# Optimization experiments

Hardware: AMD Instinct MI355X
Metric: run time of the kernel (lower is better)

Reference implementation:

```python
import jax, jax.numpy as jnp
import numpy as np

TOP_K = 2  # k in TopKGate


def setup_inputs() -> dict:
    key = jax.random.key(0)
    k1, k2, k3 = jax.random.split(key, 3)
    B, S, H, E = 4, 2048, 1024, 8
    hidden_states = jax.random.normal(k1, (B, S, H), dtype=jnp.float32)
    Wg = jax.random.normal(k2, (H, E), dtype=jnp.float32) * (H ** -0.5)
    We = jax.random.normal(k3, (E, H, H), dtype=jnp.float32) * (H ** -0.5)
    be = jnp.zeros((E, H), dtype=jnp.float32)
    return {"hidden_states": hidden_states, "Wg": Wg, "We": We, "be": be}


def reference(hidden_states, Wg, We, be):
    # hidden_states: [B, S, H]; Wg: [H, E]; We: [E, H, H]; be: [E, H]
    B, S, H = hidden_states.shape
    T = B * S
    x = hidden_states.reshape(T, H)

    # TopKGate: linear gate -> softmax -> top-k -> renormalize combine weights
    probs = jax.nn.softmax(x @ Wg, axis=-1)              # [T, E]
    top_vals, top_idx = jax.lax.top_k(probs, TOP_K)     # [T, K]
    gates = top_vals / jnp.sum(top_vals, axis=-1, keepdims=True)

    # Experts: run each token through each expert Linear, then gather top-k
    expert_out = jnp.einsum('th,ehd->etd', x, We) + be[:, None, :]  # [E, T, H]
    tok = jnp.arange(T)[:, None]                         # [T, 1]
    sel = expert_out[top_idx, tok, :]                    # [T, K, H]

    # Weighted combine over top-k experts
    out = jnp.sum(gates[..., None] * sel, axis=1)        # [T, H]
    return out.reshape(B, S, H)
```

## Files before the change

### kernel.cpp

```cpp
#include <hip/hip_runtime.h>
#include <hip/hip_bf16.h>

#define H 1024
#define NEXP 8
#define T_TOK 8192
#define CAP 8192
#define TM 128
#define TN 128
#define CNTSTRIDE 32

typedef __bf16 bf16x8 __attribute__((ext_vector_type(8)));
typedef __bf16 bf16x4 __attribute__((ext_vector_type(4)));
typedef float f32x4 __attribute__((ext_vector_type(4)));

__device__ __forceinline__ void async16(void* lds, const void* g) {
    __builtin_amdgcn_global_load_lds(
        (const __attribute__((address_space(1))) void*)g,
        (__attribute__((address_space(3))) void*)lds, 16, 0, 0);
}

__global__ __launch_bounds__(256) void moe_prep(
    const float* __restrict__ We, __bf16* __restrict__ WeT,
    const float* __restrict__ x, const float* __restrict__ Wg,
    __bf16* __restrict__ Xb, int* __restrict__ cnt,
    int* __restrict__ ltok,
    int* __restrict__ tsel, float* __restrict__ tgate) {
    __shared__ __align__(16) char smem[NEXP * H * 4];
    __shared__ __align__(16) float fin[4][8];
    __shared__ int   sE[8];
    __shared__ float sG[8];
    __shared__ int   lcnt[NEXP], lbase[NEXP], lslot[8];
    const int tid  = threadIdx.x;
    const int lane = tid & 63;
    const int wave = tid >> 6;

    if (blockIdx.x >= 2048) {
        float (*t)[65] = (float(*)[65])smem;
        const int tt = blockIdx.x - 2048;
        const int e  = tt >> 8;
        const int d0 = ((tt >> 4) & 15) * 64;
        const int h0 = (tt & 15) * 64;
        const int tx = tid & 15;
        const int ty = tid >> 4;
        const float* src = We + ((size_t)e << 20);
        __bf16* dst = WeT + ((size_t)e << 20);
#pragma unroll
        for (int p = 0; p < 4; ++p) {
            const int row = p * 16 + ty;
            const float4 v = *(const float4*)(src + (size_t)(h0 + row) * H + d0 + tx * 4);
            t[row][tx * 4 + 0] = v.x; t[row][tx * 4 + 1] = v.y;
            t[row][tx * 4 + 2] = v.z; t[row][tx * 4 + 3] = v.w;
        }
        __syncthreads();
#pragma unroll
        for (int qq = 0; qq < 2; ++qq) {
            const int q = tid + qq * 256;
            const int drow = q >> 3;
            const int seg  = q & 7;
            bf16x8 o;
#pragma unroll
            for (int i = 0; i < 8; ++i) o[i] = (__bf16)t[seg * 8 + i][drow];
            *(bf16x8*)(dst + (size_t)(d0 + drow) * H + h0 + seg * 8) = o;
        }
        return;
    }

    float (*wgT)[H] = (float(*)[H])smem;
    const int t = blockIdx.x * 4 + wave;

#pragma unroll
    for (int k = 0; k < 8; ++k) {
        const int q = k * 256 + tid;
        const float4 f = ((const float4*)Wg)[q];
        const int h  = q >> 1;
        const int e0 = (q & 1) * 4;
        wgT[e0 + 0][h] = f.x; wgT[e0 + 1][h] = f.y;
        wgT[e0 + 2][h] = f.z; wgT[e0 + 3][h] = f.w;
    }

    const float* xr = x + (size_t)t * H;
    float4 xv[4];
#pragma unroll
    for (int c = 0; c < 4; ++c)
        xv[c] = *(const float4*)(xr + c * 256 + lane * 4);

    __bf16* xbr = Xb + (size_t)t * H;
#pragma unroll
    for (int c = 0; c < 4; ++c) {
        bf16x4 xo;
        xo[0] = (__bf16)xv[c].x; xo[1] = (__bf16)xv[c].y;
        xo[2] = (__bf16)xv[c].z; xo[3] = (__bf16)xv[c].w;
        *(bf16x4*)(xbr + c * 256 + lane * 4) = xo;
    }

    __syncthreads();

    float a[NEXP];
#pragma unroll
    for (int e = 0; e < NEXP; ++e) a[e] = 0.f;
#pragma unroll
    for (int e = 0; e < NEXP; ++e) {
#pragma unroll
        for (int c = 0; c < 4; ++c) {
            const float4 wv = *(const float4*)&wgT[e][c * 256 + lane * 4];
            a[e] += xv[c].x * wv.x + xv[c].y * wv.y + xv[c].z * wv.z + xv[c].w * wv.w;
        }
    }
    if (tid < NEXP) lcnt[tid] = 0;
    __syncthreads();

    float* rw = (float*)smem + wave * 512;
#pragma unroll
    for (int e = 0; e < NEXP; ++e) rw[e * 64 + lane] = a[e];
    const int eL = lane >> 3, l8 = lane & 7;
    const float4 p0 = *(const float4*)&rw[eL * 64 + l8 * 8];
    const float4 p1 = *(const float4*)&rw[eL * 64 + l8 * 8 + 4];
    float s = ((p0.x + p0.y) + (p0.z + p0.w)) + ((p1.x + p1.y) + (p1.z + p1.w));
    s += __shfl_xor(s, 1, 64);
    s += __shfl_xor(s, 2, 64);
    s += __shfl_xor(s, 4, 64);
    if (l8 == 0) fin[wave][eL] = s;
    const float4 f0 = *(const float4*)&fin[wave][0];
    const float4 f1 = *(const float4*)&fin[wave][4];
    const float av[NEXP] = {f0.x, f0.y, f0.z, f0.w, f1.x, f1.y, f1.z, f1.w};

    int i0 = 0;
#pragma unroll
    for (int e = 1; e < NEXP; ++e) if (av[e] > av[i0]) i0 = e;
    int i1 = (i0 == 0) ? 1 : 0;
#pragma unroll
    for (int e = 0; e < NEXP; ++e) if (e != i0 && av[e] > av[i1]) i1 = e;
    const float ex = __expf(av[i1] - av[i0]);
    const float g0 = 1.f / (1.f + ex);
    const float g1 = ex / (1.f + ex);
    if (lane == 0) {
        sE[wave * 2] = i0; sE[wave * 2 + 1] = i1;
        sG[wave * 2] = g0; sG[wave * 2 + 1] = g1;
    }
    __syncthreads();
    if (tid < 8) lslot[tid] = atomicAdd(&lcnt[sE[tid]], 1);
    __syncthreads();
    if (tid < NEXP) lbase[tid] = lcnt[tid] ? atomicAdd(&cnt[tid * CNTSTRIDE], lcnt[tid]) : 0;
    __syncthreads();
    if (tid < 8) {
        const int e = sE[tid];
        const int sl = lbase[e] + lslot[tid];
        const int tt2 = blockIdx.x * 4 + (tid >> 1);
        ltok[e * CAP + sl] = tt2;
        tsel[tt2 * 2 + (tid & 1)]  = e * CAP + sl;
        tgate[tt2 * 2 + (tid & 1)] = sG[tid];
    }
}

__global__ __launch_bounds__(256) void moe_gemm(
    const __bf16* __restrict__ Xb, const __bf16* __restrict__ WeT,
    const float* __restrict__ be, const int* __restrict__ cnt,
    const int* __restrict__ ltok,
    __bf16* __restrict__ Eout) {
    const int e  = blockIdx.x & 7;
    const int nt = (blockIdx.x >> 3) & 7;
    const int mt = blockIdx.x >> 6;
    const int ne = cnt[e * CNTSTRIDE];
    const int m0 = mt * TM;
    if (m0 >= ne) return;
    const int n0 = nt * TN;
    int off = 0;
    for (int i2 = 0; i2 < e; ++i2) off += cnt[i2 * CNTSTRIDE];

    __shared__ __align__(16) __bf16 smem[4 * 4096];
    __bf16* Al  = smem;
    __bf16* Al2 = smem + 4096;
    __bf16* Bl  = smem + 8192;
    __bf16* Bl2 = smem + 12288;
    __shared__ int tokL[TM];

    const int tid = threadIdx.x;
    const int lane = tid & 63;
    const int wave = tid >> 6;

    if (tid < TM) {
        const int gi = m0 + tid;
        tokL[tid] = (gi < ne) ? ltok[e * CAP + gi] : 0;
    }
    __syncthreads();

    const __bf16* Bt = WeT + ((size_t)e << 20);
    const int qr = lane >> 4;
    const int rr = lane & 15;
    const int wr = (wave >> 1) * 64;
    const int wc = (wave & 1) * 64;

    f32x4 acc[4][4];
    const f32x4 z = {0.f, 0.f, 0.f, 0.f};
#pragma unroll
    for (int i = 0; i < 4; ++i)
#pragma unroll
        for (int j = 0; j < 4; ++j) acc[i][j] = z;

    const int c0 = tid, c1 = tid + 256;
    const int ar0 = c0 >> 2, ak0 = (((c0 & 3) ^ ((c0 >> 3) & 3)) * 8);
    const int ar1 = c1 >> 2, ak1 = (((c1 & 3) ^ ((c1 >> 3) & 3)) * 8);
    const size_t arow0 = (size_t)tokL[ar0] * H;
    const size_t arow1 = (size_t)tokL[ar1] * H;
    const size_t brow0 = (size_t)(n0 + ar0) * H;
    const size_t brow1 = (size_t)(n0 + ar1) * H;

    for (int k0 = 0; k0 < H; k0 += 64) {
        async16(&Al [c0 * 8], Xb + arow0 + k0 + ak0);
        async16(&Al [c1 * 8], Xb + arow1 + k0 + ak1);
        async16(&Al2[c0 * 8], Xb + arow0 + k0 + 32 + ak0);
        async16(&Al2[c1 * 8], Xb + arow1 + k0 + 32 + ak1);
        async16(&Bl [c0 * 8], Bt + brow0 + k0 + ak0);
        async16(&Bl [c1 * 8], Bt + brow1 + k0 + ak1);
        async16(&Bl2[c0 * 8], Bt + brow0 + k0 + 32 + ak0);
        async16(&Bl2[c1 * 8], Bt + brow1 + k0 + 32 + ak1);
        __syncthreads();
        {
            bf16x8 af[4], bfr[4];
#pragma unroll
            for (int i = 0; i < 4; ++i) {
                const int ra = wr + i * 16 + rr;
                af[i] = *(const bf16x8*)&Al[ra * 32 + ((qr ^ ((ra >> 1) & 3)) * 8)];
            }
#pragma unroll
            for (int j = 0; j < 4; ++j) {
                const int rb = wc + j * 16 + rr;
                bfr[j] = *(const bf16x8*)&Bl[rb * 32 + ((qr ^ ((rb >> 1) & 3)) * 8)];
            }
#pragma unroll
            for (int i = 0; i < 4; ++i)
#pragma unroll
                for (int j = 0; j < 4; ++j)
                    acc[i][j] = __builtin_amdgcn_mfma_f32_16x16x32_bf16(af[i], bfr[j], acc[i][j], 0, 0, 0);
        }
        {
            bf16x8 af[4], bfr[4];
#pragma unroll
            for (int i = 0; i < 4; ++i) {
                const int ra = wr + i * 16 + rr;
                af[i] = *(const bf16x8*)&Al2[ra * 32 + ((qr ^ ((ra >> 1) & 3)) * 8)];
            }
#pragma unroll
            for (int j = 0; j < 4; ++j) {
                const int rb = wc + j * 16 + rr;
                bfr[j] = *(const bf16x8*)&Bl2[rb * 32 + ((qr ^ ((rb >> 1) & 3)) * 8)];
            }
#pragma unroll
            for (int i = 0; i < 4; ++i)
#pragma unroll
                for (int j = 0; j < 4; ++j)
                    acc[i][j] = __builtin_amdgcn_mfma_f32_16x16x32_bf16(af[i], bfr[j], acc[i][j], 0, 0, 0);
        }
        __syncthreads();
    }

    float bev[4];
#pragma unroll
    for (int j = 0; j < 4; ++j) bev[j] = be[e * H + n0 + wc + j * 16 + rr];

    __bf16* Cw = smem + wave * 4096;
#pragma unroll
    for (int i = 0; i < 4; ++i) {
#pragma unroll
        for (int reg = 0; reg < 4; ++reg) {
            const int row = i * 16 + qr * 4 + reg;
            const int key = (row & 7) * 8;
#pragma unroll
            for (int j = 0; j < 4; ++j) {
                const int c = j * 16 + rr;
                Cw[row * 64 + (c ^ key)] = (__bf16)(acc[i][j][reg] + bev[j]);
            }
        }
    }
    const int lrr = lane & 7, lrg = lane >> 3;
#pragma unroll
    for (int p = 0; p < 8; ++p) {
        const int row = p * 8 + lrg;
        const int rglob = m0 + wr + row;
        if (rglob < ne) {
            const int idx8 = ((lrr ^ (row & 7)) * 8);
            const bf16x8 v = *(const bf16x8*)&Cw[row * 64 + idx8];
            *(bf16x8*)(Eout + (size_t)(off + rglob) * H + n0 + wc + lrr * 8) = v;
        }
    }
}

__global__ __launch_bounds__(256) void moe_combine(
    const __bf16* __restrict__ Eout, const int* __restrict__ cnt,
    const int* __restrict__ tsel, const float* __restrict__ tgate,
    float* __restrict__ out) {
    __shared__ int offs[NEXP];
    if (threadIdx.x < NEXP) {
        int o = 0;
        for (int i = 0; i < (int)threadIdx.x; ++i) o += cnt[i * CNTSTRIDE];
        offs[threadIdx.x] = o;
    }
    __syncthreads();
    const int wave = threadIdx.x >> 6, lane = threadIdx.x & 63;
    const int t = blockIdx.x * 4 + wave;
    const int sel0 = tsel[t * 2],  sel1 = tsel[t * 2 + 1];
    const float g0 = tgate[t * 2], g1  = tgate[t * 2 + 1];
    const int e0 = sel0 >> 13, s0 = sel0 & (CAP - 1);
    const int e1 = sel1 >> 13, s1 = sel1 & (CAP - 1);
    const __bf16* r0 = Eout + (size_t)(offs[e0] + s0) * H;
    const __bf16* r1 = Eout + (size_t)(offs[e1] + s1) * H;
    float* orow = out + (size_t)t * H;
#pragma unroll
    for (int c = 0; c < 2; ++c) {
        const int d = c * 512 + lane * 8;
        const bf16x8 a = *(const bf16x8*)(r0 + d);
        const bf16x8 b = *(const bf16x8*)(r1 + d);
        float4 o0, o1;
        o0.x = g0 * (float)a[0] + g1 * (float)b[0];
        o0.y = g0 * (float)a[1] + g1 * (float)b[1];
        o0.z = g0 * (float)a[2] + g1 * (float)b[2];
        o0.w = g0 * (float)a[3] + g1 * (float)b[3];
        o1.x = g0 * (float)a[4] + g1 * (float)b[4];
        o1.y = g0 * (float)a[5] + g1 * (float)b[5];
        o1.z = g0 * (float)a[6] + g1 * (float)b[6];
        o1.w = g0 * (float)a[7] + g1 * (float)b[7];
        *(float4*)(orow + d)     = o0;
        *(float4*)(orow + d + 4) = o1;
    }
}

extern "C" void kernel_launch(void* const* d_in, const int* in_sizes, int n_in,
                              void* d_out, int out_size, void* d_ws, size_t ws_size,
                              hipStream_t stream) {
    const float* x  = (const float*)d_in[0];
    const float* Wg = (const float*)d_in[1];
    const float* We = (const float*)d_in[2];
    const float* be = (const float*)d_in[3];
    float* out = (float*)d_out;

    char* ws = (char*)d_ws;
    __bf16* Xb   = (__bf16*)ws;
    __bf16* WeT  = (__bf16*)(ws + ((size_t)16 << 20));
    __bf16* Eout = (__bf16*)(ws + ((size_t)32 << 20));
    char*   meta = ws + ((size_t)64 << 20);
    int*    cnt  = (int*)meta;
    int*    ltok = (int*)(meta + 1024);
    int*    tsel = (int*)(meta + 1024 + (size_t)NEXP * CAP * 8);
    float*  tgat = (float*)(meta + 1024 + (size_t)NEXP * CAP * 8 + (size_t)T_TOK * 8);

    hipMemsetAsync(cnt, 0, NEXP * CNTSTRIDE * sizeof(int), stream);

    moe_prep<<<4096, 256, 0, stream>>>(We, WeT, x, Wg, Xb, cnt, ltok, tsel, tgat);
    moe_gemm<<<8 * 8 * (T_TOK / TM), 256, 0, stream>>>(Xb, WeT, be, cnt, ltok, Eout);
    moe_combine<<<T_TOK / 4, 256, 0, stream>>>(Eout, cnt, tsel, tgat, out);
}
```

Before: 182.2 us.

## Pipeline expert GEMM K-loop with triple-buffered async LDS loads

Replaces the load-then-sync-then-compute K loop (64-wide steps, two sync barriers per step) with a three-stage ring of 32-wide K tiles. Global-to-LDS loads for tile k+2 are issued while tile k is computed, and explicit vmcnt waits with a single raw barrier per step replace __syncthreads. This is meant to hide global load latency behind MFMA work. In exchange it uses more LDS (48KB vs 32KB), which may reduce occupancy, and it doubles the number of loop iterations and barriers.

```diff
diff --git a/kernel.cpp b/kernel.cpp
--- a/kernel.cpp
+++ b/kernel.cpp
@@ -18,6 +18,13 @@
         (const __attribute__((address_space(1))) void*)g,
         (__attribute__((address_space(3))) void*)lds, 16, 0, 0);
 }
+
+__device__ __forceinline__ void bar() {
+    asm volatile("" ::: "memory");
+    __builtin_amdgcn_s_barrier();
+    asm volatile("" ::: "memory");
+}
+#define VMCNT(n) asm volatile("s_waitcnt vmcnt(" #n ")" ::: "memory")
 
 __global__ __launch_bounds__(256) void moe_prep(
     const float* __restrict__ We, __bf16* __restrict__ WeT,
@@ -167,11 +174,7 @@
     int off = 0;
     for (int i2 = 0; i2 < e; ++i2) off += cnt[i2 * CNTSTRIDE];
 
-    __shared__ __align__(16) __bf16 smem[4 * 4096];
-    __bf16* Al  = smem;
-    __bf16* Al2 = smem + 4096;
-    __bf16* Bl  = smem + 8192;
-    __bf16* Bl2 = smem + 12288;
+    __shared__ __align__(16) __bf16 smem[3 * 8192];
     __shared__ int tokL[TM];
 
     const int tid = threadIdx.x;
@@ -205,27 +208,36 @@
     const size_t brow0 = (size_t)(n0 + ar0) * H;
     const size_t brow1 = (size_t)(n0 + ar1) * H;
 
-    for (int k0 = 0; k0 < H; k0 += 64) {
-        async16(&Al [c0 * 8], Xb + arow0 + k0 + ak0);
-        async16(&Al [c1 * 8], Xb + arow1 + k0 + ak1);
-        async16(&Al2[c0 * 8], Xb + arow0 + k0 + 32 + ak0);
-        async16(&Al2[c1 * 8], Xb + arow1 + k0 + 32 + ak1);
-        async16(&Bl [c0 * 8], Bt + brow0 + k0 + ak0);
-        async16(&Bl [c1 * 8], Bt + brow1 + k0 + ak1);
-        async16(&Bl2[c0 * 8], Bt + brow0 + k0 + 32 + ak0);
-        async16(&Bl2[c1 * 8], Bt + brow1 + k0 + 32 + ak1);
-        __syncthreads();
+#define STAGE(base, k0)                                              \
+    do {                                                             \
+        async16((base) + c0 * 8,        Xb + arow0 + (k0) + ak0);    \
+        async16((base) + c1 * 8,        Xb + arow1 + (k0) + ak1);    \
+        async16((base) + 4096 + c0 * 8, Bt + brow0 + (k0) + ak0);    \
+        async16((base) + 4096 + c1 * 8, Bt + brow1 + (k0) + ak1);    \
+    } while (0)
+
+    __bf16* b0 = smem;
+    __bf16* b1 = smem + 8192;
+    __bf16* b2 = smem + 16384;
+
+    STAGE(b0, 0);
+    STAGE(b1, 32);
+
+    for (int kt = 0; kt < 32; ++kt) {
+        if (kt < 31) { VMCNT(4); } else { VMCNT(0); }
+        bar();
+        if (kt < 30) STAGE(b2, (kt + 2) * 32);
         {
             bf16x8 af[4], bfr[4];
 #pragma unroll
             for (int i = 0; i < 4; ++i) {
                 const int ra = wr + i * 16 + rr;
-                af[i] = *(const bf16x8*)&Al[ra * 32 + ((qr ^ ((ra >> 1) & 3)) * 8)];
+                af[i] = *(const bf16x8*)&b0[ra * 32 + ((qr ^ ((ra >> 1) & 3)) * 8)];
             }
 #pragma unroll
             for (int j = 0; j < 4; ++j) {
                 const int rb = wc + j * 16 + rr;
-                bfr[j] = *(const bf16x8*)&Bl[rb * 32 + ((qr ^ ((rb >> 1) & 3)) * 8)];
+                bfr[j] = *(const bf16x8*)&b0[4096 + rb * 32 + ((qr ^ ((rb >> 1) & 3)) * 8)];
             }
 #pragma unroll
             for (int i = 0; i < 4; ++i)
@@ -233,26 +245,11 @@
                 for (int j = 0; j < 4; ++j)
                     acc[i][j] = __builtin_amdgcn_mfma_f32_16x16x32_bf16(af[i], bfr[j], acc[i][j], 0, 0, 0);
         }
-        {
-            bf16x8 af[4], bfr[4];
-#pragma unroll
-            for (int i = 0; i < 4; ++i) {
-                const int ra = wr + i * 16 + rr;
-                af[i] = *(const bf16x8*)&Al2[ra * 32 + ((qr ^ ((ra >> 1) & 3)) * 8)];
-            }
-#pragma unroll
-            for (int j = 0; j < 4; ++j) {
-                const int rb = wc + j * 16 + rr;
-                bfr[j] = *(const bf16x8*)&Bl2[rb * 32 + ((qr ^ ((rb >> 1) & 3)) * 8)];
-            }
-#pragma unroll
-            for (int i = 0; i < 4; ++i)
-#pragma unroll
-                for (int j = 0; j < 4; ++j)
-                    acc[i][j] = __builtin_amdgcn_mfma_f32_16x16x32_bf16(af[i], bfr[j], acc[i][j], 0, 0, 0);
-        }
-        __syncthreads();
-    }
+        __bf16* tmp = b0; b0 = b1; b1 = b2; b2 = tmp;
+    }
+#undef STAGE
+
+    __syncthreads();
 
     float bev[4];
 #pragma unroll
```

New measurement: 192.1 us. 1.05x slower.
